# Optimization experiments

Hardware: AMD Instinct MI355X
Metric: run time of the kernel (lower is better)

## Reference

```python
import jax, jax.numpy as jnp
from jax import lax
import numpy as np

DIM = 1024
HID = 1536
K = 4
C_CONST = 8.0


def setup_inputs() -> dict:
    key = jax.random.key(0)
    ks = jax.random.split(key, 12)
    d, h = DIM, HID
    x = jax.random.normal(ks[0], (4, 4096, d), dtype=jnp.float32)
    Wg = jax.random.normal(ks[1], (h, d), dtype=jnp.float32) * d ** -0.5
    Wi = jax.random.normal(ks[2], (h, d), dtype=jnp.float32) * d ** -0.5
    conv_w = jax.random.normal(ks[3], (h, 1, K), dtype=jnp.float32) * (1.0 / K) ** 0.5
    conv_b = jax.random.normal(ks[4], (h,), dtype=jnp.float32) * 0.02
    lru_Wi = jax.random.normal(ks[5], (h, h), dtype=jnp.float32) * h ** -0.5
    lru_bi = jnp.zeros((h,), dtype=jnp.float32)
    lru_Wg = jax.random.normal(ks[6], (h, h), dtype=jnp.float32) * h ** -0.5
    lru_bg = jnp.zeros((h,), dtype=jnp.float32)
    lam = jnp.linspace(-4.323, -9.0, h, dtype=jnp.float32)
    Wo = jax.random.normal(ks[7], (d, h), dtype=jnp.float32) * h ** -0.5
    return {"x": x, "Wg": Wg, "Wi": Wi, "conv_w": conv_w, "conv_b": conv_b,
            "lru_Wi": lru_Wi, "lru_bi": lru_bi, "lru_Wg": lru_Wg, "lru_bg": lru_bg,
            "lam": lam, "Wo": Wo}


def _hawk_forward(x, Wg, Wi, conv_w, conv_b, lru_Wi, lru_bi, lru_Wg, lru_bg, lam, Wo):
    H = Wg.shape[0]
    k = conv_w.shape[-1]
    gate = jnp.einsum('bsd,hd->bsh', x, Wg)        # [B,S,H]
    u = jnp.einsum('bsd,hd->bsh', x, Wi)           # [B,S,H]
    # causal depthwise conv1d (torch pads k-1 both sides then slices [:S] == left-pad k-1)
    y = lax.conv_general_dilated(
        u.transpose(0, 2, 1), conv_w, window_strides=(1,),
        padding=[(k - 1, 0)], dimension_numbers=('NCH', 'OIH', 'NCH'),
        feature_group_count=H) + conv_b[None, :, None]
    y = y.transpose(0, 2, 1)                        # [B,S,H]
    # RG_LRU
    ig = jax.nn.sigmoid(jnp.einsum('bsh,gh->bsg', y, lru_Wi) + lru_bi)
    rg = jax.nn.sigmoid(jnp.einsum('bsh,gh->bsg', y, lru_Wg) + lru_bg)
    alpha = jnp.exp(-C_CONST * jax.nn.softplus(lam) * rg)
    beta = jnp.sqrt(1.0 - alpha ** 2 + 1e-6)
    xbeta = beta * ig * y
    # diagonal linear recurrence h_t = alpha_t * h_{t-1} + xbeta_t via associative scan
    def combine(c1, c2):
        a1, b1 = c1
        a2, b2 = c2
        return a1 * a2, a2 * b1 + b2
    _, h = lax.associative_scan(combine, (alpha, xbeta), axis=1)
    return jnp.einsum('bsh,dh->bsd', jax.nn.gelu(gate, approximate=False) * h, Wo)


def reference(x, Wg, Wi, conv_w, conv_b, lru_Wi, lru_bi, lru_Wg, lru_bg, lam, Wo):
    return _hawk_forward(x, Wg, Wi, conv_w, conv_b, lru_Wi, lru_bi, lru_Wg, lru_bg, lam, Wo)
```

## Files before the change

kernel.cpp:

```cpp
#include <hip/hip_runtime.h>
#include <hip/hip_bf16.h>
#include <math.h>

#define B_  4
#define S_  4096
#define D_  1024
#define H_  1536
#define M_  (B_*S_)
#define CCONST 8.0f

#define CL  128
#define NC  (S_/CL)

#define BM 128
#define BN 128
#define BK 32

using bf16x8 = __attribute__((ext_vector_type(8))) short;
using f32x4  = __attribute__((ext_vector_type(4))) float;
using u16x8  = __attribute__((ext_vector_type(8))) unsigned short;

__device__ __forceinline__ float bf2f(unsigned short u){
    union{unsigned i; float f;} v; v.i = ((unsigned)u)<<16; return v.f;
}
__device__ __forceinline__ unsigned short f2bf(float f){
    union{float f; unsigned i;} v; v.f = f;
    unsigned r = v.i + 0x7fffu + ((v.i>>16)&1u);
    return (unsigned short)(r>>16);
}

#define GLOAD16(gp, lp) __builtin_amdgcn_global_load_lds( \
    (const __attribute__((address_space(1))) void*)(gp),  \
    (__attribute__((address_space(3))) void*)(lp), 16, 0, 0)

__global__ void cast_bf16_kernel(const float* __restrict__ in,
                                 unsigned short* __restrict__ out, int n8)
{
    int i = blockIdx.x*blockDim.x + threadIdx.x;
    if (i >= n8) return;
    const float4* p = reinterpret_cast<const float4*>(in + (size_t)i*8);
    float4 a = p[0], b = p[1];
    u16x8 o;
    o[0]=f2bf(a.x); o[1]=f2bf(a.y); o[2]=f2bf(a.z); o[3]=f2bf(a.w);
    o[4]=f2bf(b.x); o[5]=f2bf(b.y); o[6]=f2bf(b.z); o[7]=f2bf(b.w);
    *reinterpret_cast<u16x8*>(out + (size_t)i*8) = o;
}

template<int MODE>
__global__ __launch_bounds__(256) void gemm_bt(
    const unsigned short* __restrict__ A, const unsigned short* __restrict__ Bw,
    void* __restrict__ out, int M, int N, int K)
{
    __shared__ alignas(16) unsigned short As[2][BM*BK];
    __shared__ alignas(16) unsigned short Bs[2][BN*BK];
    const int tid = threadIdx.x, lane = tid&63, wid = tid>>6;
    const int row0 = blockIdx.x*BM, col0 = blockIdx.y*BN;
    const int wr = (wid>>1)*64, wc = (wid&1)*64;
    const int lr = lane&15, kg = lane>>4;

    const int eb0 = (wid*64)*8,  eb1 = ((256 + wid*64))*8;
    const int le0 = eb0 + lane*8, le1 = eb1 + lane*8;
    const int ar0 = le0>>5, ac0 = le0&31;
    const int ar1 = le1>>5, ac1 = le1&31;

    auto stage = [&](int buf, int k0){
        GLOAD16(&A [(size_t)(row0+ar0)*K + (k0+ac0)], &As[buf][eb0]);
        GLOAD16(&Bw[(size_t)(col0+ar0)*K + (k0+ac0)], &Bs[buf][eb0]);
        GLOAD16(&A [(size_t)(row0+ar1)*K + (k0+ac1)], &As[buf][eb1]);
        GLOAD16(&Bw[(size_t)(col0+ar1)*K + (k0+ac1)], &Bs[buf][eb1]);
    };

    f32x4 acc[4][4];
    #pragma unroll
    for (int m=0;m<4;m++)
        #pragma unroll
        for (int n=0;n<4;n++) acc[m][n] = (f32x4){0.f,0.f,0.f,0.f};

    const int nk = K/BK;
    stage(0, 0);
    __syncthreads();
    int cur = 0;
    for (int t=0; t<nk; ++t){
        if (t+1 < nk) stage(cur^1, (t+1)*BK);
        bf16x8 af[4], bfr[4];
        #pragma unroll
        for (int m=0;m<4;m++) af[m]  = *(const bf16x8*)&As[cur][(wr + m*16 + lr)*BK + kg*8];
        #pragma unroll
        for (int n=0;n<4;n++) bfr[n] = *(const bf16x8*)&Bs[cur][(wc + n*16 + lr)*BK + kg*8];
        #pragma unroll
        for (int m=0;m<4;m++)
            #pragma unroll
            for (int n=0;n<4;n++)
                acc[m][n] = __builtin_amdgcn_mfma_f32_16x16x32_bf16(af[m], bfr[n], acc[m][n], 0,0,0);
        __syncthreads();
        cur ^= 1;
    }

    #pragma unroll
    for (int n=0;n<4;n++){
        int c = col0 + wc + n*16 + lr;
        #pragma unroll
        for (int m=0;m<4;m++){
            int rbase = row0 + wr + m*16 + kg*4;
            #pragma unroll
            for (int j=0;j<4;j++){
                float v = acc[m][n][j];
                size_t idx = (size_t)(rbase+j)*N + c;
                if constexpr (MODE==0){
                    ((unsigned short*)out)[idx] = f2bf(v);
                } else {
                    ((float*)out)[idx] = v;
                }
            }
        }
    }
}

template<int EPI>
__global__ __launch_bounds__(256) void gemm_dual(
    const unsigned short* __restrict__ Aall,
    const unsigned short* __restrict__ B1, const unsigned short* __restrict__ B2,
    unsigned short* __restrict__ O1, unsigned short* __restrict__ O2,
    const float* __restrict__ bi, const float* __restrict__ bg,
    const float* __restrict__ lam,
    int N, int K)
{
    __shared__ alignas(16) unsigned short As [2][BM*BK];
    __shared__ alignas(16) unsigned short Bs1[2][BN*BK];
    __shared__ alignas(16) unsigned short Bs2[2][BN*BK];
    const int tid = threadIdx.x, lane = tid&63, wid = tid>>6;
    const int row0 = blockIdx.x*BM, col0 = blockIdx.y*BN;
    const int wr = (wid>>1)*64, wc = (wid&1)*64;
    const int lr = lane&15, kg = lane>>4;

    const int eb0 = (wid*64)*8,  eb1 = ((256 + wid*64))*8;
    const int le0 = eb0 + lane*8, le1 = eb1 + lane*8;
    const int ar0 = le0>>5, ac0 = le0&31;
    const int ar1 = le1>>5, ac1 = le1&31;

    auto stage = [&](int buf, int k0){
        GLOAD16(&Aall[(size_t)(row0+ar0)*K + (k0+ac0)], &As [buf][eb0]);
        GLOAD16(&B1  [(size_t)(col0+ar0)*K + (k0+ac0)], &Bs1[buf][eb0]);
        GLOAD16(&B2  [(size_t)(col0+ar0)*K + (k0+ac0)], &Bs2[buf][eb0]);
        GLOAD16(&Aall[(size_t)(row0+ar1)*K + (k0+ac1)], &As [buf][eb1]);
        GLOAD16(&B1  [(size_t)(col0+ar1)*K + (k0+ac1)], &Bs1[buf][eb1]);
        GLOAD16(&B2  [(size_t)(col0+ar1)*K + (k0+ac1)], &Bs2[buf][eb1]);
    };

    f32x4 a1[4][4], a2[4][4];
    #pragma unroll
    for (int m=0;m<4;m++)
        #pragma unroll
        for (int n=0;n<4;n++){ a1[m][n]=(f32x4){0.f,0.f,0.f,0.f}; a2[m][n]=(f32x4){0.f,0.f,0.f,0.f}; }

    const int nk = K/BK;
    stage(0, 0);
    __syncthreads();
    int cur = 0;
    for (int t=0; t<nk; ++t){
        if (t+1 < nk) stage(cur^1, (t+1)*BK);
        bf16x8 af[4], b1f[4], b2f[4];
        #pragma unroll
        for (int m=0;m<4;m++) af[m]  = *(const bf16x8*)&As [cur][(wr + m*16 + lr)*BK + kg*8];
        #pragma unroll
        for (int n=0;n<4;n++){ b1f[n] = *(const bf16x8*)&Bs1[cur][(wc + n*16 + lr)*BK + kg*8];
                               b2f[n] = *(const bf16x8*)&Bs2[cur][(wc + n*16 + lr)*BK + kg*8]; }
        #pragma unroll
        for (int m=0;m<4;m++)
            #pragma unroll
            for (int n=0;n<4;n++){
                a1[m][n] = __builtin_amdgcn_mfma_f32_16x16x32_bf16(af[m], b1f[n], a1[m][n], 0,0,0);
                a2[m][n] = __builtin_amdgcn_mfma_f32_16x16x32_bf16(af[m], b2f[n], a2[m][n], 0,0,0);
            }
        __syncthreads();
        cur ^= 1;
    }

    #pragma unroll
    for (int n=0;n<4;n++){
        int c = col0 + wc + n*16 + lr;
        float bic = 0.f, msp = 0.f, bgc = 0.f;
        if constexpr (EPI==1){
            bic = bi[c]; bgc = bg[c];
            msp = -CCONST * log1pf(expf(lam[c]));
        }
        #pragma unroll
        for (int m=0;m<4;m++){
            int rbase = row0 + wr + m*16 + kg*4;
            #pragma unroll
            for (int j=0;j<4;j++){
                size_t idx = (size_t)(rbase+j)*N + c;
                float z1 = a1[m][n][j];
                float z2 = a2[m][n][j];
                if constexpr (EPI==0){
                    float g = 0.5f*z1*(1.0f + erff(z1*0.70710678118654752f));
                    O1[idx] = f2bf(g);
                    O2[idx] = f2bf(z2);
                } else {
                    float zi = z1 + bic;
                    float zg = z2 + bgc;
                    float ig = 1.f/(1.f+expf(-zi));
                    float rg = 1.f/(1.f+expf(-zg));
                    float lav = msp*rg;
                    float a  = expf(lav);
                    float bt = sqrtf(1.f - a*a + 1e-6f);
                    float y  = bf2f(Aall[idx]);
                    O1[idx] = f2bf(lav);
                    O2[idx] = f2bf(bt*ig*y);
                }
            }
        }
    }
}

__global__ void conv_kernel(const unsigned short* __restrict__ U,
                            const float* __restrict__ W,
                            const float* __restrict__ Cb,
                            unsigned short* __restrict__ Y)
{
    int gid = blockIdx.x*blockDim.x + threadIdx.x;
    int hc = gid % (H_/8); int m = gid / (H_/8);
    int s = m & (S_-1);
    int h0 = hc*8;
    size_t base = (size_t)m*H_ + h0;
    float acc[8];
    #pragma unroll
    for (int j=0;j<8;j++) acc[j] = Cb[h0+j];
    #pragma unroll
    for (int i=0;i<4;i++){
        int ss = s - 3 + i;
        if (ss < 0) continue;
        u16x8 uv = *reinterpret_cast<const u16x8*>(&U[(size_t)(m-3+i)*H_ + h0]);
        #pragma unroll
        for (int j=0;j<8;j++) acc[j] += W[(h0+j)*4 + i] * bf2f(uv[j]);
    }
    u16x8 o;
    #pragma unroll
    for (int j=0;j<8;j++) o[j] = f2bf(acc[j]);
    *reinterpret_cast<u16x8*>(&Y[base]) = o;
}

__global__ void scan1_kernel(const unsigned short* __restrict__ la,
                             const unsigned short* __restrict__ xbeta,
                             float* __restrict__ Ac, float* __restrict__ Bc)
{
    int h = blockIdx.x*blockDim.x + threadIdx.x;
    int b = blockIdx.y, c = blockIdx.z;
    size_t base = ((size_t)b*S_ + (size_t)c*CL)*H_ + h;
    float sa = 0.f, Bv = 0.f;
    for (int t=0;t<CL;t++){
        float l = bf2f(la   [base + (size_t)t*H_]);
        float x = bf2f(xbeta[base + (size_t)t*H_]);
        Bv = expf(l)*Bv + x;
        sa += l;
    }
    size_t o = ((size_t)c*B_ + b)*H_ + h;
    Ac[o] = expf(sa); Bc[o] = Bv;
}

__global__ void scan2_kernel(const float* __restrict__ Ac, const float* __restrict__ Bc,
                             float* __restrict__ Hin)
{
    int idx = blockIdx.x*blockDim.x + threadIdx.x;
    int b = idx / H_, h = idx % H_;
    float hcur = 0.f;
    for (int c=0;c<NC;c++){
        size_t o = ((size_t)c*B_ + b)*H_ + h;
        Hin[o] = hcur;
        hcur = Ac[o]*hcur + Bc[o];
    }
}

__global__ void scan3_kernel(const unsigned short* __restrict__ la,
                             const unsigned short* __restrict__ xbeta,
                             const float* __restrict__ Hin,
                             const unsigned short* __restrict__ Gg,
                             unsigned short* __restrict__ Vb)
{
    int h = blockIdx.x*blockDim.x + threadIdx.x;
    int b = blockIdx.y, c = blockIdx.z;
    size_t base = ((size_t)b*S_ + (size_t)c*CL)*H_ + h;
    float hcur = Hin[((size_t)c*B_ + b)*H_ + h];
    for (int t=0;t<CL;t++){
        size_t o = base + (size_t)t*H_;
        float l = bf2f(la[o]);
        float x = bf2f(xbeta[o]);
        hcur = expf(l)*hcur + x;
        float g = bf2f(Gg[o]);
        Vb[o] = f2bf(g*hcur);
    }
}

extern "C" void kernel_launch(void* const* d_in, const int* in_sizes, int n_in,
                              void* d_out, int out_size, void* d_ws, size_t ws_size,
                              hipStream_t stream)
{
    const float* x      = (const float*)d_in[0];
    const float* Wg     = (const float*)d_in[1];
    const float* Wi     = (const float*)d_in[2];
    const float* conv_w = (const float*)d_in[3];
    const float* conv_b = (const float*)d_in[4];
    const float* lru_Wi = (const float*)d_in[5];
    const float* lru_bi = (const float*)d_in[6];
    const float* lru_Wg = (const float*)d_in[7];
    const float* lru_bg = (const float*)d_in[8];
    const float* lam    = (const float*)d_in[9];
    const float* Wo     = (const float*)d_in[10];
    float* out = (float*)d_out;

    const size_t BY16 = (size_t)M_*H_*2;
    char* w = (char*)d_ws;
    unsigned short* xb    = (unsigned short*)w;
    unsigned short* la    = (unsigned short*)w;  w += BY16;
    unsigned short* ggb   = (unsigned short*)w;  w += BY16;
    unsigned short* ub    = (unsigned short*)w;  w += BY16;
    unsigned short* xbeta = (unsigned short*)w;  w += BY16;
    unsigned short* wgb   = (unsigned short*)w;  w += (size_t)H_*D_*2;
    unsigned short* wib   = (unsigned short*)w;  w += (size_t)H_*D_*2;
    unsigned short* wliB  = (unsigned short*)w;  w += (size_t)H_*H_*2;
    unsigned short* wlgB  = (unsigned short*)w;  w += (size_t)H_*H_*2;
    unsigned short* wob   = (unsigned short*)w;  w += (size_t)D_*H_*2;
    float* Ac  = (float*)w; w += (size_t)NC*B_*H_*4;
    float* Bc  = (float*)w; w += (size_t)NC*B_*H_*4;
    float* Hin = (float*)w; w += (size_t)NC*B_*H_*4;
    unsigned short* yb = (unsigned short*)d_out;
    unsigned short* vb = ub;

    size_t need = (size_t)(w - (char*)d_ws);
    if (ws_size < need) return;

    cast_bf16_kernel<<<(M_*D_/8)/256,   256, 0, stream>>>(x,      xb,   M_*D_/8);
    cast_bf16_kernel<<<(H_*D_/8)/256,   256, 0, stream>>>(Wg,     wgb,  H_*D_/8);
    cast_bf16_kernel<<<(H_*D_/8)/256,   256, 0, stream>>>(Wi,     wib,  H_*D_/8);
    cast_bf16_kernel<<<(H_*H_/8)/256,   256, 0, stream>>>(lru_Wi, wliB, H_*H_/8);
    cast_bf16_kernel<<<(H_*H_/8)/256,   256, 0, stream>>>(lru_Wg, wlgB, H_*H_/8);
    cast_bf16_kernel<<<(D_*H_/8)/256,   256, 0, stream>>>(Wo,     wob,  D_*H_/8);

    gemm_dual<0><<<dim3(M_/BM, H_/BN), 256, 0, stream>>>(
        xb, wgb, wib, ggb, ub, nullptr, nullptr, nullptr, H_, D_);

    conv_kernel<<<(M_*(H_/8))/256, 256, 0, stream>>>(ub, conv_w, conv_b, yb);

    gemm_dual<1><<<dim3(M_/BM, H_/BN), 256, 0, stream>>>(
        yb, wliB, wlgB, la, xbeta, lru_bi, lru_bg, lam, H_, H_);

    scan1_kernel<<<dim3(H_/256, B_, NC), 256, 0, stream>>>(la, xbeta, Ac, Bc);
    scan2_kernel<<<(B_*H_)/256, 256, 0, stream>>>(Ac, Bc, Hin);
    scan3_kernel<<<dim3(H_/256, B_, NC), 256, 0, stream>>>(la, xbeta, Hin, ggb, vb);

    gemm_bt<2><<<dim3(M_/BM, D_/BN), 256, 0, stream>>>(vb, wob, out, M_, D_, H_);
}
```

Before: 1.093 ms.

## Triple-buffer GEMM LDS tiles with counted vmcnt waits and single barrier

Both GEMM kernels move from double to triple LDS buffering, keeping two K-tiles of global-to-LDS loads in flight. The full __syncthreads is replaced by a partial s_waitcnt vmcnt plus a raw s_barrier, and the barrier now sits between the LDS fragment reads and the MFMA block, so each iteration has one sync instead of waiting on every outstanding load. The aim is to hide global load latency better. In exchange LDS use grows by half, which may lower occupancy (the dual kernel goes to about 72KB), and correctness now depends on the hand-counted vmcnt values.

```diff
diff --git a/kernel.cpp b/kernel.cpp
--- a/kernel.cpp
+++ b/kernel.cpp
@@ -32,6 +32,14 @@
 #define GLOAD16(gp, lp) __builtin_amdgcn_global_load_lds( \
     (const __attribute__((address_space(1))) void*)(gp),  \
     (__attribute__((address_space(3))) void*)(lp), 16, 0, 0)
+
+#define WAITBAR(vm_asm)                                   \
+    do {                                                  \
+        asm volatile(vm_asm ::: "memory");                \
+        __builtin_amdgcn_sched_barrier(0);                \
+        __builtin_amdgcn_s_barrier();                     \
+        __builtin_amdgcn_sched_barrier(0);                \
+    } while (0)
 
 __global__ void cast_bf16_kernel(const float* __restrict__ in,
                                  unsigned short* __restrict__ out, int n8)
@@ -51,8 +59,8 @@
     const unsigned short* __restrict__ A, const unsigned short* __restrict__ Bw,
     void* __restrict__ out, int M, int N, int K)
 {
-    __shared__ alignas(16) unsigned short As[2][BM*BK];
-    __shared__ alignas(16) unsigned short Bs[2][BN*BK];
+    __shared__ alignas(16) unsigned short As[3][BM*BK];
+    __shared__ alignas(16) unsigned short Bs[3][BN*BK];
     const int tid = threadIdx.x, lane = tid&63, wid = tid>>6;
     const int row0 = blockIdx.x*BM, col0 = blockIdx.y*BN;
     const int wr = (wid>>1)*64, wc = (wid&1)*64;
@@ -78,22 +86,29 @@
 
     const int nk = K/BK;
     stage(0, 0);
-    __syncthreads();
+    stage(1, BK);
+    WAITBAR("s_waitcnt vmcnt(4)");
     int cur = 0;
     for (int t=0; t<nk; ++t){
-        if (t+1 < nk) stage(cur^1, (t+1)*BK);
         bf16x8 af[4], bfr[4];
         #pragma unroll
         for (int m=0;m<4;m++) af[m]  = *(const bf16x8*)&As[cur][(wr + m*16 + lr)*BK + kg*8];
         #pragma unroll
         for (int n=0;n<4;n++) bfr[n] = *(const bf16x8*)&Bs[cur][(wc + n*16 + lr)*BK + kg*8];
+        int nxt = cur+1==3 ? 0 : cur+1;
+        int nnx = nxt+1==3 ? 0 : nxt+1;
+        if (t+2 < nk){
+            stage(nnx, (t+2)*BK);
+            WAITBAR("s_waitcnt vmcnt(4) lgkmcnt(0)");
+        } else {
+            WAITBAR("s_waitcnt vmcnt(0) lgkmcnt(0)");
+        }
         #pragma unroll
         for (int m=0;m<4;m++)
             #pragma unroll
             for (int n=0;n<4;n++)
                 acc[m][n] = __builtin_amdgcn_mfma_f32_16x16x32_bf16(af[m], bfr[n], acc[m][n], 0,0,0);
-        __syncthreads();
-        cur ^= 1;
+        cur = nxt;
     }
 
     #pragma unroll
@@ -125,9 +140,9 @@
     const float* __restrict__ lam,
     int N, int K)
 {
-    __shared__ alignas(16) unsigned short As [2][BM*BK];
-    __shared__ alignas(16) unsigned short Bs1[2][BN*BK];
-    __shared__ alignas(16) unsigned short Bs2[2][BN*BK];
+    __shared__ alignas(16) unsigned short As [3][BM*BK];
+    __shared__ alignas(16) unsigned short Bs1[3][BN*BK];
+    __shared__ alignas(16) unsigned short Bs2[3][BN*BK];
     const int tid = threadIdx.x, lane = tid&63, wid = tid>>6;
     const int row0 = blockIdx.x*BM, col0 = blockIdx.y*BN;
     const int wr = (wid>>1)*64, wc = (wid&1)*64;
@@ -155,16 +170,24 @@
 
     const int nk = K/BK;
     stage(0, 0);
-    __syncthreads();
+    stage(1, BK);
+    WAITBAR("s_waitcnt vmcnt(6)");
     int cur = 0;
     for (int t=0; t<nk; ++t){
-        if (t+1 < nk) stage(cur^1, (t+1)*BK);
         bf16x8 af[4], b1f[4], b2f[4];
         #pragma unroll
         for (int m=0;m<4;m++) af[m]  = *(const bf16x8*)&As [cur][(wr + m*16 + lr)*BK + kg*8];
         #pragma unroll
         for (int n=0;n<4;n++){ b1f[n] = *(const bf16x8*)&Bs1[cur][(wc + n*16 + lr)*BK + kg*8];
                                b2f[n] = *(const bf16x8*)&Bs2[cur][(wc + n*16 + lr)*BK + kg*8]; }
+        int nxt = cur+1==3 ? 0 : cur+1;
+        int nnx = nxt+1==3 ? 0 : nxt+1;
+        if (t+2 < nk){
+            stage(nnx, (t+2)*BK);
+            WAITBAR("s_waitcnt vmcnt(6) lgkmcnt(0)");
+        } else {
+            WAITBAR("s_waitcnt vmcnt(0) lgkmcnt(0)");
+        }
         #pragma unroll
         for (int m=0;m<4;m++)
             #pragma unroll
@@ -172,8 +195,7 @@
                 a1[m][n] = __builtin_amdgcn_mfma_f32_16x16x32_bf16(af[m], b1f[n], a1[m][n], 0,0,0);
                 a2[m][n] = __builtin_amdgcn_mfma_f32_16x16x32_bf16(af[m], b2f[n], a2[m][n], 0,0,0);
             }
-        __syncthreads();
-        cur ^= 1;
+        cur = nxt;
     }
 
     #pragma unroll
```

Result: faster. 957.2 us (-12.5%).
